# Kernel optimization log

Hardware: AMD Instinct MI355X
Metric: run time of the kernel (lower is better)

The kernel has to match this reference:

```python
import jax, jax.numpy as jnp
import numpy as np

D_MODEL = 1024
D_INNER = 2048      # expand * d_model
D_STATE = 64
HEADDIM = 128
NHEADS = 16         # d_inner // headdim
D_CONV = 4
CHUNK = 256
D_IN_PROJ = 2 * D_INNER + 2 * D_STATE + NHEADS   # 4240 (ngroups=1)
CONV_DIM = D_INNER + 2 * D_STATE                 # 2176
EPS = 1e-5


def setup_inputs() -> dict:
    key = jax.random.key(0)
    ks = jax.random.split(key, 8)
    B, L = 2, 4096
    u = jax.random.normal(ks[0], (B, L, D_MODEL), jnp.float32)
    in_proj_w = jax.random.normal(ks[1], (D_IN_PROJ, D_MODEL), jnp.float32) / np.sqrt(D_MODEL)
    conv_w = jax.random.uniform(ks[2], (CONV_DIM, D_CONV), jnp.float32, -0.5, 0.5)
    conv_b = jnp.zeros((CONV_DIM,), jnp.float32)
    # dt_bias init exactly as in the module: inv-softplus of dt ~ logU(1e-3, 1e-1)
    dt0 = jnp.exp(jax.random.uniform(ks[3], (NHEADS,), jnp.float32) * (np.log(0.1) - np.log(0.001)) + np.log(0.001))
    dt_bias = dt0 + jnp.log(-jnp.expm1(-dt0))
    A_log = jnp.log(jax.random.uniform(ks[4], (NHEADS,), jnp.float32, 1.0, 16.0))
    Dp = jnp.ones((NHEADS,), jnp.float32)
    norm_w = jnp.ones((D_INNER,), jnp.float32)
    out_proj_w = jax.random.normal(ks[5], (D_MODEL, D_INNER), jnp.float32) / np.sqrt(D_INNER)
    return dict(u=u, in_proj_w=in_proj_w, conv_w=conv_w, conv_b=conv_b, dt_bias=dt_bias,
                A_log=A_log, Dp=Dp, norm_w=norm_w, out_proj_w=out_proj_w)


def _ssd(x, dt, A, Bm, Cm, Dp):
    # Chunked selective state-space scan (mamba_chunk_scan_combined semantics).
    # x: [b,l,h,p], dt: [b,l,h] (already softplus'd), A: [h] (negative), Bm/Cm: [b,l,n]
    b, l, h, p = x.shape
    n = Bm.shape[-1]
    nc = l // CHUNK
    xc = x.reshape(b, nc, CHUNK, h, p)
    dtc = dt.reshape(b, nc, CHUNK, h)
    Bc = Bm.reshape(b, nc, CHUNK, n)
    Cc = Cm.reshape(b, nc, CHUNK, n)
    a = dtc * A                       # [b,c,q,h], a <= 0
    acum = jnp.cumsum(a, axis=2)      # within-chunk cumulative log-decay
    # ---- intra-chunk (causal, attention-like) ----
    scores = jnp.einsum('bcqn,bckn->bcqk', Cc, Bc)
    diff = acum[:, :, :, None, :] - acum[:, :, None, :, :]        # [b,c,q,k,h]
    mask = jnp.tril(jnp.ones((CHUNK, CHUNK), bool))[None, None, :, :, None]
    decay = jnp.exp(jnp.where(mask, diff, -jnp.inf))
    M = scores[..., None] * decay * dtc[:, :, None, :, :]         # [b,c,q,k,h]
    y_diag = jnp.einsum('bcqkh,bckhp->bcqhp', M, xc)
    # ---- per-chunk end states ----
    decay_states = jnp.exp(acum[:, :, -1:, :] - acum)             # [b,c,q,h]
    states = jnp.einsum('bcqh,bcqn,bcqhp->bchpn', dtc * decay_states, Bc, xc)
    # ---- inter-chunk recurrence (scan over nc chunks) ----
    chunk_decay = jnp.exp(acum[:, :, -1, :])                      # [b,c,h]
    def step(s, inp):
        st, cd = inp
        return cd[:, :, None, None] * s + st, s                   # emit state BEFORE this chunk
    init = jnp.zeros((b, h, p, n), x.dtype)
    _, prev = jax.lax.scan(step, init, (states.transpose(1, 0, 2, 3, 4), chunk_decay.transpose(1, 0, 2)))
    prev = prev.transpose(1, 0, 2, 3, 4)                          # [b,c,h,p,n]
    y_off = jnp.einsum('bcqn,bchpn,bcqh->bcqhp', Cc, prev, jnp.exp(acum))
    y = y_diag + y_off + xc * Dp[None, None, None, :, None]
    return y.reshape(b, l, h, p)


def _forward(u, in_proj_w, conv_w, conv_b, dt_bias, A_log, Dp, norm_w, out_proj_w):
    b, l, _ = u.shape
    zxbct = jnp.einsum('bld,ed->ble', u, in_proj_w)
    z = zxbct[..., :D_INNER]
    xBC = zxbct[..., D_INNER:D_INNER + CONV_DIM]
    dt = zxbct[..., D_INNER + CONV_DIM:]
    dt = jax.nn.softplus(dt + dt_bias)                            # [b,l,h]
    # causal depthwise conv1d (padding d_conv-1, truncated to seq_len) + SiLU
    xp = jnp.pad(xBC, ((0, 0), (D_CONV - 1, 0), (0, 0)))
    conv_out = conv_b
    for w in range(D_CONV):
        conv_out = conv_out + xp[:, w:w + l, :] * conv_w[:, w]
    xBC = jax.nn.silu(conv_out)
    x = xBC[..., :D_INNER]
    Bm = xBC[..., D_INNER:D_INNER + D_STATE]
    Cm = xBC[..., D_INNER + D_STATE:]
    A = -jnp.exp(A_log)
    y = _ssd(x.reshape(b, l, NHEADS, HEADDIM), dt, A, Bm, Cm, Dp)
    y = y.reshape(b, l, D_INNER)
    # RMSNormGated (norm_before_gate=False): gate first, then RMSNorm
    y = y * jax.nn.silu(z)
    y = y * jax.lax.rsqrt(jnp.mean(y * y, axis=-1, keepdims=True) + EPS) * norm_w
    return jnp.einsum('ble,de->bld', y, out_proj_w)


def reference(u, in_proj_w, conv_w, conv_b, dt_bias, A_log, Dp, norm_w, out_proj_w):
    return _forward(u, in_proj_w, conv_w, conv_b, dt_bias, A_log, Dp, norm_w, out_proj_w)
```

## Files before the change

### kernel.cpp

```cpp
#include <hip/hip_runtime.h>
#include <hip/hip_bf16.h>
#include <cstdint>
#include <cstddef>

#define D_MODEL   1024
#define D_INNER   2048
#define D_STATE   64
#define HEADDIM   128
#define NHEADS    16
#define D_CONV    4
#define CHUNK     256
#define D_IN_PROJ 4240
#define ZPAD      4352
#define CONV_DIM  2176
#define NB        2
#define LEN       4096
#define NC        16
#define MROWS     (NB*LEN)

typedef __hip_bfloat16 bf16;
typedef __bf16 bf16x8 __attribute__((ext_vector_type(8)));
typedef float  f32x4  __attribute__((ext_vector_type(4)));
typedef unsigned short us4 __attribute__((ext_vector_type(4)));

__device__ __forceinline__ float fsilu(float x){ return x / (1.f + __expf(-x)); }
__device__ __forceinline__ float toF(float x){ return x; }
__device__ __forceinline__ float toF(bf16 x){ return __bfloat162float(x); }

__device__ __forceinline__ unsigned short f2bs(float v){
  return __bfloat16_as_ushort(__float2bfloat16(v));
}
__device__ __forceinline__ void store4(bf16* p, f32x4 v){
  us4 o; o[0]=f2bs(v[0]); o[1]=f2bs(v[1]); o[2]=f2bs(v[2]); o[3]=f2bs(v[3]);
  *(us4*)p = o;
}
__device__ __forceinline__ void store4(float* p, f32x4 v){
  *(f32x4*)p = v;
}

__device__ __forceinline__ void gload_lds16(const void* g, void* l){
  __builtin_amdgcn_global_load_lds(
     (const __attribute__((address_space(1))) unsigned int*)(uintptr_t)g,
     (__attribute__((address_space(3))) unsigned int*)(uintptr_t)l, 16, 0, 0);
}

template<typename TC>
__global__ __launch_bounds__(256) void k_gemm_db(
    const bf16* __restrict__ A, int lda,
    const bf16* __restrict__ B, int ldb,
    TC* __restrict__ C, int ldc, int K)
{
  __shared__ __align__(16) __bf16 As[2][128*64];
  __shared__ __align__(16) __bf16 Bs[2][128*64];
  const int tid  = threadIdx.x;
  const int w    = tid >> 6, l = tid & 63;
  const int quad = l >> 4, lq = l & 15;
  const int wm   = (w & 1)*64, wn = (w >> 1)*64;
  const int m0 = blockIdx.x*128, n0 = blockIdx.y*128;

  const int rs = w*8 + (l >> 3);
  const int cs = ((l & 7) ^ (l >> 3)) * 8;
  const bf16* Ag = A + (size_t)(m0 + rs)*lda + cs;
  const bf16* Bg = B + (size_t)(n0 + rs)*ldb + cs;

  auto stage = [&](int t, int buf){
    const int k0 = t*64;
    #pragma unroll
    for (int j=0;j<4;j++){
      gload_lds16(Ag + (size_t)j*32*lda + k0, (char*)&As[buf][0] + (j*32 + w*8)*128);
      gload_lds16(Bg + (size_t)j*32*ldb + k0, (char*)&Bs[buf][0] + (j*32 + w*8)*128);
    }
  };

  f32x4 acc[4][4] = {};

  stage(0, 0);
  const int NT = K >> 6;
  for (int t = 0; t < NT; ++t){
    const int cur = t & 1;
    if (t+1 < NT){
      stage(t+1, cur^1);
      asm volatile("s_waitcnt vmcnt(8)" ::: "memory");
    } else {
      asm volatile("s_waitcnt vmcnt(0)" ::: "memory");
    }
    asm volatile("s_barrier" ::: "memory");

    const char* Ab = (const char*)&As[cur][0];
    const char* Bb = (const char*)&Bs[cur][0];
    #pragma unroll
    for (int s=0;s<2;s++){
      const int slot = ((s*4 + quad) ^ (lq & 7)) << 4;
      bf16x8 af[4], bfr[4];
      #pragma unroll
      for (int tm=0;tm<4;tm++)
        af[tm]  = *(const bf16x8*)(Ab + (wm + lq + tm*16)*128 + slot);
      #pragma unroll
      for (int tn=0;tn<4;tn++)
        bfr[tn] = *(const bf16x8*)(Bb + (wn + lq + tn*16)*128 + slot);
      #pragma unroll
      for (int tm=0;tm<4;tm++)
        #pragma unroll
        for (int tn=0;tn<4;tn++)
          acc[tm][tn] = __builtin_amdgcn_mfma_f32_16x16x32_bf16(bfr[tn], af[tm], acc[tm][tn], 0,0,0);
    }
    asm volatile("s_barrier" ::: "memory");
  }

  #pragma unroll
  for (int tm = 0; tm < 4; tm++){
    int r = m0 + wm + tm*16 + lq;
    #pragma unroll
    for (int tn = 0; tn < 4; tn++){
      int cb = n0 + wn + tn*16 + quad*4;
      store4(&C[(size_t)r*ldc + cb], acc[tm][tn]);
    }
  }
}

#define NU4  (MROWS*D_MODEL/4)
#define NW14 (ZPAD*D_MODEL/4)
#define NW24 (D_MODEL*D_INNER/4)
__global__ __launch_bounds__(256) void k_convert(
    const float* __restrict__ u, const float* __restrict__ Win,
    const float* __restrict__ Wout, const float* __restrict__ norm_w,
    bf16* __restrict__ ub, bf16* __restrict__ Wb_in, bf16* __restrict__ Wb_out){
  int i4 = blockIdx.x*256 + threadIdx.x;
  if (i4 < NU4){
    float4 v = ((const float4*)u)[i4];
    us4 o = {f2bs(v.x), f2bs(v.y), f2bs(v.z), f2bs(v.w)};
    ((us4*)ub)[i4] = o;
  } else if (i4 < NU4 + NW14){
    int j = i4 - NU4;
    int r = j >> 8;
    float4 v = make_float4(0.f,0.f,0.f,0.f);
    if (r < D_IN_PROJ) v = ((const float4*)Win)[j];
    us4 o = {f2bs(v.x), f2bs(v.y), f2bs(v.z), f2bs(v.w)};
    ((us4*)Wb_in)[j] = o;
  } else {
    int j = i4 - NU4 - NW14;
    float4 v = ((const float4*)Wout)[j];
    float4 nw = ((const float4*)norm_w)[j & 511];
    us4 o = {f2bs(v.x*nw.x), f2bs(v.y*nw.y), f2bs(v.z*nw.z), f2bs(v.w*nw.w)};
    ((us4*)Wb_out)[j] = o;
  }
}

__global__ __launch_bounds__(256) void k_dt(
    const bf16* __restrict__ zxbct, const float* __restrict__ dt_bias,
    const float* __restrict__ A_log, float* __restrict__ dt_t,
    float* __restrict__ acum_t, float* __restrict__ cd_t){
  int bid = blockIdx.x;
  int h = bid & 15, c = (bid>>4)&15, b = bid>>8;
  int q = threadIdx.x;
  size_t m = (size_t)(b*NC + c)*CHUNK + q;
  float x = toF(zxbct[m*ZPAD + (D_INNER + CONV_DIM) + h]) + dt_bias[h];
  float dtv = (x > 20.f) ? x : log1pf(__expf(x));
  float Ah = -__expf(A_log[h]);
  float a = dtv * Ah;
  __shared__ float sb[CHUNK];
  sb[q] = a;
  __syncthreads();
  #pragma unroll
  for (int off=1; off<CHUNK; off<<=1){
    float t = (q >= off) ? sb[q-off] : 0.f;
    __syncthreads();
    sb[q] += t;
    __syncthreads();
  }
  float ac = sb[q];
  size_t o = ((size_t)(b*NHEADS+h))*LEN + c*CHUNK + q;
  dt_t[o]   = dtv;
  acum_t[o] = ac;
  if (q == CHUNK-1) cd_t[(b*NHEADS+h)*NC + c] = __expf(ac);
}

__global__ __launch_bounds__(256) void k_conv(
    const bf16* __restrict__ zxbct, const float* __restrict__ conv_w,
    const float* __restrict__ conv_b, bf16* __restrict__ xbc){
  __shared__ __align__(16) __bf16 xs[67*64];
  __shared__ __align__(16) float  ws[64*4];
  __shared__ float bs[64];
  const int tid = threadIdx.x;
  const int cq = tid & 7;
  const int tm = tid >> 3;
  const int c0 = blockIdx.x*64;
  const int m0 = blockIdx.y*64;
  {
    int g = m0 - 3 + tm; if (g < 0) g = 0;
    *(bf16x8*)&xs[tm*64 + cq*8] =
        *(const bf16x8*)(zxbct + (size_t)g*ZPAD + D_INNER + c0 + cq*8);
    int g2 = m0 - 3 + tm + 32;
    *(bf16x8*)&xs[(tm+32)*64 + cq*8] =
        *(const bf16x8*)(zxbct + (size_t)g2*ZPAD + D_INNER + c0 + cq*8);
    if (tid < 24){
      int r3 = 64 + (tid >> 3);
      int g3 = m0 - 3 + r3;
      *(bf16x8*)&xs[r3*64 + cq*8] =
          *(const bf16x8*)(zxbct + (size_t)g3*ZPAD + D_INNER + c0 + cq*8);
    }
  }
  if (tid < 64)      *(float4*)&ws[tid*4] = *(const float4*)(conv_w + (size_t)(c0+tid)*4);
  else if (tid < 128) bs[tid-64] = conv_b[c0 + tid - 64];
  __syncthreads();

  #pragma unroll
  for (int rr=0; rr<2; rr++){
    const int r = tm + rr*32;
    const int m = m0 + r;
    const int l = m & (LEN-1);
    float acc[8];
    #pragma unroll
    for (int j=0;j<8;j++) acc[j] = bs[cq*8+j];
    #pragma unroll
    for (int w=0; w<D_CONV; w++){
      if (l - (D_CONV-1) + w >= 0){
        bf16x8 v = *(const bf16x8*)&xs[(r+w)*64 + cq*8];
        #pragma unroll
        for (int j=0;j<8;j++) acc[j] += (float)v[j] * ws[(cq*8+j)*4 + w];
      }
    }
    bf16x8 o;
    #pragma unroll
    for (int j=0;j<8;j++) o[j] = (__bf16)fsilu(acc[j]);
    *(bf16x8*)(xbc + (size_t)m*CONV_DIM + c0 + cq*8) = o;
  }
}

__global__ __launch_bounds__(256,2) void k_states(
    const bf16* __restrict__ xbc, const float* __restrict__ acum_t,
    const float* __restrict__ dt_t, float* __restrict__ states)
{
  const int bid = blockIdx.x;
  const int h = bid & 15, c = (bid>>4)&15, b = bid>>8;
  const int z = b*NC + c;
  const int tid = threadIdx.x;
  const int w = tid >> 6, l = tid & 63;
  const int quad = l >> 4, lq = l & 15;

  __shared__ __align__(16) __bf16 xsT[2][128*72];
  __shared__ __align__(16) __bf16 bts[2][64*72];

  const float* acum = acum_t + ((size_t)(b*NHEADS+h))*LEN + c*CHUNK;
  const float* dtc  = dt_t   + ((size_t)(b*NHEADS+h))*LEN + c*CHUNK;
  const float alast = acum[CHUNK-1];
  const bf16* xrow = xbc + (size_t)z*CHUNK*CONV_DIM + h*HEADDIM;
  const bf16* Brow = xbc + (size_t)z*CHUNK*CONV_DIM + D_INNER;

  f32x4 Sst[2][4] = {};

  auto stage = [&](int t, int buf){
    const int k0 = t*64;
    const bf16* xr = xrow + (size_t)(k0+l)*CONV_DIM;
    #pragma unroll
    for (int pass=0; pass<4; pass++){
      int pb = w*8 + pass*32;
      bf16x8 v = *(const bf16x8*)(xr + pb);
      #pragma unroll
      for (int j=0;j<8;j++) xsT[buf][(pb+j)*72 + l] = v[j];
    }
    float wl = dtc[k0+l] * __expf(alast - acum[k0+l]);
    const bf16* br = Brow + (size_t)(k0+l)*CONV_DIM;
    #pragma unroll
    for (int pass=0; pass<2; pass++){
      int nb = w*8 + pass*32;
      bf16x8 v = *(const bf16x8*)(br + nb);
      #pragma unroll
      for (int j=0;j<8;j++) bts[buf][(nb+j)*72 + l] = (__bf16)((float)v[j] * wl);
    }
  };

  stage(0, 0);
  for (int t = 0; t < 4; t++){
    const int buf = t & 1;
    __syncthreads();
    if (t < 3) stage(t+1, buf^1);
    #pragma unroll
    for (int s=0;s<2;s++){
      bf16x8 a2[2];
      #pragma unroll
      for (int mi=0;mi<2;mi++)
        a2[mi] = *(const bf16x8*)&xsT[buf][(w*32 + mi*16 + lq)*72 + s*32 + quad*8];
      #pragma unroll
      for (int ni=0;ni<4;ni++){
        bf16x8 bb = *(const bf16x8*)&bts[buf][(ni*16+lq)*72 + s*32 + quad*8];
        #pragma unroll
        for (int mi=0;mi<2;mi++)
          Sst[mi][ni] = __builtin_amdgcn_mfma_f32_16x16x32_bf16(bb, a2[mi], Sst[mi][ni], 0,0,0);
      }
    }
  }

  float* so = states + (size_t)bid*HEADDIM*D_STATE;
  #pragma unroll
  for (int mi=0;mi<2;mi++){
    int pp = w*32 + mi*16 + lq;
    #pragma unroll
    for (int ni=0;ni<4;ni++)
      store4(&so[pp*D_STATE + ni*16 + quad*4], Sst[mi][ni]);
  }
}

__global__ __launch_bounds__(256) void k_scan(
    const float* __restrict__ states, const float* __restrict__ cd_t,
    bf16* __restrict__ prevb){
  int b = blockIdx.x >> 4, h = blockIdx.x & 15;
  int pt = blockIdx.y;
  int tid = threadIdx.x;
  float carry[4] = {0.f,0.f,0.f,0.f};
  for (int c=0;c<NC;c++){
    size_t base = ((size_t)(b*256 + c*16 + h))*HEADDIM*D_STATE + (size_t)pt*1024;
    float cd = cd_t[(b*NHEADS+h)*NC + c];
    #pragma unroll
    for (int i=0;i<4;i++){
      size_t idx = base + (size_t)i*256 + tid;
      prevb[idx] = __float2bfloat16(carry[i]);
      carry[i] = carry[i]*cd + states[idx];
    }
  }
}

__global__ __launch_bounds__(256,2) void k_fused(
    const bf16* __restrict__ xbc, const float* __restrict__ acum_t,
    const float* __restrict__ dt_t, const float* __restrict__ Dp,
    const bf16* __restrict__ prevb, bf16* __restrict__ y)
{
  const int bid = blockIdx.x;
  const int h = bid & 15, c = (bid>>4)&15, b = bid>>8;
  const int z = b*NC + c;
  const int tid = threadIdx.x;
  const int w = tid >> 6, l = tid & 63;
  const int quad = l >> 4, lq = l & 15;

  __shared__ __align__(16) __bf16 xsT[2][128*72];
  __shared__ __align__(16) __bf16 Ms[4][32*40];
  __shared__ float acs[CHUNK], dts[CHUNK];

  const float* acum = acum_t + ((size_t)(b*NHEADS+h))*LEN + c*CHUNK;
  const float* dtc  = dt_t   + ((size_t)(b*NHEADS+h))*LEN + c*CHUNK;
  acs[tid] = acum[tid];
  dts[tid] = dtc[tid];

  const bf16* xrow = xbc + (size_t)z*CHUNK*CONV_DIM + h*HEADDIM;
  const bf16* Brow = xbc + (size_t)z*CHUNK*CONV_DIM + D_INNER;
  const bf16* Crow = xbc + (size_t)z*CHUNK*CONV_DIM + D_INNER + D_STATE;
  const bf16* pv   = prevb + (size_t)bid*HEADDIM*D_STATE;
  const float Dph = Dp[h];
  const int j0 = w, j1 = 7 - w;

  f32x4 Yacc[2][2][8] = {};

  auto stage = [&](int t, int buf){
    const bf16* xr = xrow + (size_t)(t*64+l)*CONV_DIM;
    #pragma unroll
    for (int pass=0; pass<4; pass++){
      int pb = w*8 + pass*32;
      bf16x8 v = *(const bf16x8*)(xr + pb);
      #pragma unroll
      for (int j=0;j<8;j++) xsT[buf][(pb+j)*72 + l] = v[j];
    }
  };

  stage(0, 0);
  __syncthreads();

  #pragma unroll
  for (int s=0;s<2;s++){
    bf16x8 bp[8];
    #pragma unroll
    for (int pn=0;pn<8;pn++)
      bp[pn] = *(const bf16x8*)(pv + (pn*16+lq)*D_STATE + s*32 + quad*8);
    #pragma unroll
    for (int half=0; half<2; half++){
      const int j = half ? j1 : j0;
      #pragma unroll
      for (int qm=0;qm<2;qm++){
        int row = j*32 + qm*16 + lq;
        float e = __expf(acs[row]);
        bf16x8 a = *(const bf16x8*)(Crow + (size_t)row*CONV_DIM + s*32 + quad*8);
        bf16x8 ae;
        #pragma unroll
        for (int jj=0;jj<8;jj++) ae[jj] = (__bf16)((float)a[jj] * e);
        #pragma unroll
        for (int pn=0;pn<8;pn++)
          Yacc[half][qm][pn] = __builtin_amdgcn_mfma_f32_16x16x32_bf16(bp[pn], ae, Yacc[half][qm][pn], 0,0,0);
      }
    }
  }

  for (int t = 0; t < 4; t++){
    const int buf = t & 1;
    if (t > 0) __syncthreads();
    if (t < 3) stage(t+1, buf^1);

    #pragma unroll
    for (int half=0; half<2; half++){
      const int j = half ? j1 : j0;
      if (2*t > j) continue;
      const int qbase = j*32;
      bf16x8 cf[2][2];
      #pragma unroll
      for (int s=0;s<2;s++)
        #pragma unroll
        for (int qm=0;qm<2;qm++)
          cf[s][qm] = *(const bf16x8*)(Crow + (size_t)(qbase+qm*16+lq)*CONV_DIM + s*32 + quad*8);
      #pragma unroll
      for (int kk=0; kk<2; kk++){
        const int kh = 2*t + kk;
        if (kh > j) continue;
        const int kb32  = kk*32;
        const int kbase = kh*32;
        f32x4 Sacc[2][2] = {};
        #pragma unroll
        for (int s=0;s<2;s++){
          bf16x8 bfk[2];
          #pragma unroll
          for (int kn=0;kn<2;kn++)
            bfk[kn] = *(const bf16x8*)(Brow + (size_t)(kbase+kn*16+lq)*CONV_DIM + s*32 + quad*8);
          #pragma unroll
          for (int kn=0;kn<2;kn++)
            #pragma unroll
            for (int qm=0;qm<2;qm++)
              Sacc[kn][qm] = __builtin_amdgcn_mfma_f32_16x16x32_bf16(bfk[kn], cf[s][qm], Sacc[kn][qm], 0,0,0);
        }
        #pragma unroll
        for (int qm=0;qm<2;qm++){
          int ql = qbase + qm*16 + lq;
          float aq = acs[ql];
          #pragma unroll
          for (int kn=0;kn<2;kn++){
            us4 o;
            #pragma unroll
            for (int i=0;i<4;i++){
              int kl = kbase + kn*16 + quad*4 + i;
              float v = Sacc[kn][qm][i] * __expf(aq - acs[kl]) * dts[kl];
              v = (kl < ql) ? v : ((kl == ql) ? v + Dph : 0.f);
              o[i] = f2bs(v);
            }
            *(us4*)&Ms[w][(qm*16+lq)*40 + kn*16 + quad*4] = o;
          }
        }
        asm volatile("s_waitcnt lgkmcnt(0)" ::: "memory");
        #pragma unroll
        for (int qm=0;qm<2;qm++){
          bf16x8 am = *(const bf16x8*)&Ms[w][(qm*16+lq)*40 + quad*8];
          #pragma unroll
          for (int pn=0;pn<8;pn++){
            bf16x8 bp = *(const bf16x8*)&xsT[buf][(pn*16+lq)*72 + kb32 + quad*8];
            Yacc[half][qm][pn] = __builtin_amdgcn_mfma_f32_16x16x32_bf16(bp, am, Yacc[half][qm][pn], 0,0,0);
          }
        }
      }
    }
  }

  bf16* yrow = y + (size_t)z*CHUNK*D_INNER + h*HEADDIM;
  #pragma unroll
  for (int half=0; half<2; half++){
    const int j = half ? j1 : j0;
    #pragma unroll
    for (int qm=0;qm<2;qm++){
      int q = j*32 + qm*16 + lq;
      #pragma unroll
      for (int pn=0;pn<8;pn++)
        store4(&yrow[(size_t)q*D_INNER + pn*16 + quad*4], Yacc[half][qm][pn]);
    }
  }
}

__global__ __launch_bounds__(256) void k_gatenorm(
    const bf16* __restrict__ zxbct, bf16* __restrict__ y){
  int m = blockIdx.x;
  int e0 = threadIdx.x*8;
  bf16x8 zv = *(const bf16x8*)(zxbct + (size_t)m*ZPAD + e0);
  bf16x8 yv = *(const bf16x8*)(y + (size_t)m*D_INNER + e0);
  float v[8]; float ss = 0.f;
  #pragma unroll
  for (int j=0;j<8;j++){
    float val = (float)yv[j] * fsilu((float)zv[j]);
    v[j] = val; ss += val*val;
  }
  #pragma unroll
  for (int off=32; off>0; off>>=1) ss += __shfl_down(ss, off, 64);
  __shared__ float red[4];
  if ((threadIdx.x & 63) == 0) red[threadIdx.x >> 6] = ss;
  __syncthreads();
  float tot = red[0]+red[1]+red[2]+red[3];
  float r = rsqrtf(tot * (1.f/D_INNER) + 1e-5f);
  bf16x8 o;
  #pragma unroll
  for (int j=0;j<8;j++) o[j] = (__bf16)(v[j] * r);
  *(bf16x8*)(y + (size_t)m*D_INNER + e0) = o;
}

extern "C" void kernel_launch(void* const* d_in, const int* in_sizes, int n_in,
                              void* d_out, int out_size, void* d_ws, size_t ws_size,
                              hipStream_t stream) {
  const float* u         = (const float*)d_in[0];
  const float* in_proj_w = (const float*)d_in[1];
  const float* conv_w    = (const float*)d_in[2];
  const float* conv_b    = (const float*)d_in[3];
  const float* dt_bias   = (const float*)d_in[4];
  const float* A_log     = (const float*)d_in[5];
  const float* Dp        = (const float*)d_in[6];
  const float* norm_w    = (const float*)d_in[7];
  const float* out_proj_w= (const float*)d_in[8];
  float* out = (float*)d_out;

  char* p = (char*)d_ws;
  auto alloc = [&](size_t bytes){ char* r = p; p += (bytes + 255) & ~size_t(255); return r; };
  bf16*  zxbct = (bf16*) alloc((size_t)MROWS*ZPAD*2);
  bf16*  xbc   = (bf16*) alloc((size_t)MROWS*CONV_DIM*2);
  bf16*  y     = (bf16*) alloc((size_t)MROWS*D_INNER*2);
  bf16*  ub    = (bf16*) alloc((size_t)MROWS*D_MODEL*2);
  bf16*  Wb_in = (bf16*) alloc((size_t)ZPAD*D_MODEL*2);
  bf16*  Wb_out= (bf16*) alloc((size_t)D_MODEL*D_INNER*2);
  float* dt_t  = (float*)alloc((size_t)NB*NHEADS*LEN*4);
  float* acum_t= (float*)alloc((size_t)NB*NHEADS*LEN*4);
  float* cd_t  = (float*)alloc((size_t)NB*NHEADS*NC*4);
  float* states= (float*)ub;
  bf16*  prevb = (bf16*)Wb_in;

  dim3 blk(256);
  k_convert<<<dim3((NU4+NW14+NW24)/256), blk, 0, stream>>>(
      u, in_proj_w, out_proj_w, norm_w, ub, Wb_in, Wb_out);

  k_gemm_db<bf16><<<dim3(64, 34), blk, 0, stream>>>(
      ub, D_MODEL, Wb_in, D_MODEL, zxbct, ZPAD, D_MODEL);

  k_dt    <<<dim3(NB*NC*NHEADS), blk, 0, stream>>>(zxbct, dt_bias, A_log, dt_t, acum_t, cd_t);
  k_conv  <<<dim3(CONV_DIM/64, MROWS/64), blk, 0, stream>>>(zxbct, conv_w, conv_b, xbc);
  k_states<<<dim3(NB*NC*NHEADS), blk, 0, stream>>>(xbc, acum_t, dt_t, states);
  k_scan  <<<dim3(NB*NHEADS, 8), blk, 0, stream>>>(states, cd_t, prevb);
  k_fused <<<dim3(NB*NC*NHEADS), blk, 0, stream>>>(xbc, acum_t, dt_t, Dp, prevb, y);
  k_gatenorm<<<dim3(MROWS), blk, 0, stream>>>(zxbct, y);

  k_gemm_db<float><<<dim3(64, 8), blk, 0, stream>>>(
      y, D_INNER, Wb_out, D_INNER, out, D_MODEL, D_INNER);
}
```

Before: 344.4 us.

## Run GEMM tiles with eight waves per block and hoist C fragments in fused SSD kernel

Both GEMMs now run with 512 threads per block instead of 256. Each wave computes a 64x32 sub-tile instead of 64x64, and the LDS staging is reindexed so each thread issues four 16-byte global-to-LDS loads per K step. The goal is more waves for latency hiding and fewer accumulator registers per wave. Separately, the fused SSD kernel loads its C-matrix fragments once into registers and reuses them across the state pass and every intra-chunk step, instead of reloading them from global memory each time. This costs more resident registers in that kernel.

```diff
diff --git a/kernel.cpp b/kernel.cpp
--- a/kernel.cpp
+++ b/kernel.cpp
@@ -45,7 +45,7 @@
 }
 
 template<typename TC>
-__global__ __launch_bounds__(256) void k_gemm_db(
+__global__ __launch_bounds__(512) void k_gemm_8w(
     const bf16* __restrict__ A, int lda,
     const bf16* __restrict__ B, int ldb,
     TC* __restrict__ C, int ldc, int K)
@@ -55,24 +55,27 @@
   const int tid  = threadIdx.x;
   const int w    = tid >> 6, l = tid & 63;
   const int quad = l >> 4, lq = l & 15;
-  const int wm   = (w & 1)*64, wn = (w >> 1)*64;
+  const int wm   = (w & 1)*64;
+  const int wn   = (w >> 1)*32;
   const int m0 = blockIdx.x*128, n0 = blockIdx.y*128;
 
-  const int rs = w*8 + (l >> 3);
-  const int cs = ((l & 7) ^ (l >> 3)) * 8;
-  const bf16* Ag = A + (size_t)(m0 + rs)*lda + cs;
-  const bf16* Bg = B + (size_t)(n0 + rs)*ldb + cs;
+  const int sr = tid >> 3;
+  const int sc = ((tid & 7) ^ (sr & 7)) * 8;
+  const bf16* Ag = A + (size_t)(m0 + sr)*lda + sc;
+  const bf16* Bg = B + (size_t)(n0 + sr)*ldb + sc;
+  const int sdo = w*1024;
 
   auto stage = [&](int t, int buf){
     const int k0 = t*64;
-    #pragma unroll
-    for (int j=0;j<4;j++){
-      gload_lds16(Ag + (size_t)j*32*lda + k0, (char*)&As[buf][0] + (j*32 + w*8)*128);
-      gload_lds16(Bg + (size_t)j*32*ldb + k0, (char*)&Bs[buf][0] + (j*32 + w*8)*128);
-    }
+    char* ab = (char*)&As[buf][0] + sdo;
+    char* bb = (char*)&Bs[buf][0] + sdo;
+    gload_lds16(Ag + k0,                  ab);
+    gload_lds16(Ag + (size_t)64*lda + k0, ab + 8192);
+    gload_lds16(Bg + k0,                  bb);
+    gload_lds16(Bg + (size_t)64*ldb + k0, bb + 8192);
   };
 
-  f32x4 acc[4][4] = {};
+  f32x4 acc[4][2] = {};
 
   stage(0, 0);
   const int NT = K >> 6;
@@ -80,7 +83,7 @@
     const int cur = t & 1;
     if (t+1 < NT){
       stage(t+1, cur^1);
-      asm volatile("s_waitcnt vmcnt(8)" ::: "memory");
+      asm volatile("s_waitcnt vmcnt(4)" ::: "memory");
     } else {
       asm volatile("s_waitcnt vmcnt(0)" ::: "memory");
     }
@@ -90,18 +93,18 @@
     const char* Bb = (const char*)&Bs[cur][0];
     #pragma unroll
     for (int s=0;s<2;s++){
-      const int slot = ((s*4 + quad) ^ (lq & 7)) << 4;
-      bf16x8 af[4], bfr[4];
+      const int slot = (((s*4 + quad) ^ (lq & 7)) << 4);
+      bf16x8 af[4], bfr[2];
       #pragma unroll
       for (int tm=0;tm<4;tm++)
-        af[tm]  = *(const bf16x8*)(Ab + (wm + lq + tm*16)*128 + slot);
-      #pragma unroll
-      for (int tn=0;tn<4;tn++)
-        bfr[tn] = *(const bf16x8*)(Bb + (wn + lq + tn*16)*128 + slot);
+        af[tm]  = *(const bf16x8*)(Ab + (wm + tm*16 + lq)*128 + slot);
+      #pragma unroll
+      for (int tn=0;tn<2;tn++)
+        bfr[tn] = *(const bf16x8*)(Bb + (wn + tn*16 + lq)*128 + slot);
       #pragma unroll
       for (int tm=0;tm<4;tm++)
         #pragma unroll
-        for (int tn=0;tn<4;tn++)
+        for (int tn=0;tn<2;tn++)
           acc[tm][tn] = __builtin_amdgcn_mfma_f32_16x16x32_bf16(bfr[tn], af[tm], acc[tm][tn], 0,0,0);
     }
     asm volatile("s_barrier" ::: "memory");
@@ -111,7 +114,7 @@
   for (int tm = 0; tm < 4; tm++){
     int r = m0 + wm + tm*16 + lq;
     #pragma unroll
-    for (int tn = 0; tn < 4; tn++){
+    for (int tn = 0; tn < 2; tn++){
       int cb = n0 + wn + tn*16 + quad*4;
       store4(&C[(size_t)r*ldc + cb], acc[tm][tn]);
     }
@@ -362,6 +365,18 @@
   };
 
   stage(0, 0);
+
+  bf16x8 cfh[2][2][2];
+  #pragma unroll
+  for (int half=0; half<2; half++){
+    const int j = half ? j1 : j0;
+    #pragma unroll
+    for (int s=0;s<2;s++)
+      #pragma unroll
+      for (int qm=0;qm<2;qm++)
+        cfh[half][s][qm] = *(const bf16x8*)(Crow + (size_t)(j*32+qm*16+lq)*CONV_DIM + s*32 + quad*8);
+  }
+
   __syncthreads();
 
   #pragma unroll
@@ -377,7 +392,7 @@
       for (int qm=0;qm<2;qm++){
         int row = j*32 + qm*16 + lq;
         float e = __expf(acs[row]);
-        bf16x8 a = *(const bf16x8*)(Crow + (size_t)row*CONV_DIM + s*32 + quad*8);
+        bf16x8 a = cfh[half][s][qm];
         bf16x8 ae;
         #pragma unroll
         for (int jj=0;jj<8;jj++) ae[jj] = (__bf16)((float)a[jj] * e);
@@ -398,12 +413,6 @@
       const int j = half ? j1 : j0;
       if (2*t > j) continue;
       const int qbase = j*32;
-      bf16x8 cf[2][2];
-      #pragma unroll
-      for (int s=0;s<2;s++)
-        #pragma unroll
-        for (int qm=0;qm<2;qm++)
-          cf[s][qm] = *(const bf16x8*)(Crow + (size_t)(qbase+qm*16+lq)*CONV_DIM + s*32 + quad*8);
       #pragma unroll
       for (int kk=0; kk<2; kk++){
         const int kh = 2*t + kk;
@@ -421,7 +430,7 @@
           for (int kn=0;kn<2;kn++)
             #pragma unroll
             for (int qm=0;qm<2;qm++)
-              Sacc[kn][qm] = __builtin_amdgcn_mfma_f32_16x16x32_bf16(bfk[kn], cf[s][qm], Sacc[kn][qm], 0,0,0);
+              Sacc[kn][qm] = __builtin_amdgcn_mfma_f32_16x16x32_bf16(bfk[kn], cfh[half][s][qm], Sacc[kn][qm], 0,0,0);
         }
         #pragma unroll
         for (int qm=0;qm<2;qm++){
@@ -525,7 +534,7 @@
   k_convert<<<dim3((NU4+NW14+NW24)/256), blk, 0, stream>>>(
       u, in_proj_w, out_proj_w, norm_w, ub, Wb_in, Wb_out);
 
-  k_gemm_db<bf16><<<dim3(64, 34), blk, 0, stream>>>(
+  k_gemm_8w<bf16><<<dim3(64, 34), dim3(512), 0, stream>>>(
       ub, D_MODEL, Wb_in, D_MODEL, zxbct, ZPAD, D_MODEL);
 
   k_dt    <<<dim3(NB*NC*NHEADS), blk, 0, stream>>>(zxbct, dt_bias, A_log, dt_t, acum_t, cd_t);
@@ -535,6 +544,6 @@
   k_fused <<<dim3(NB*NC*NHEADS), blk, 0, stream>>>(xbc, acum_t, dt_t, Dp, prevb, y);
   k_gatenorm<<<dim3(MROWS), blk, 0, stream>>>(zxbct, y);
 
-  k_gemm_db<float><<<dim3(64, 8), blk, 0, stream>>>(
+  k_gemm_8w<float><<<dim3(64, 8), dim3(512), 0, stream>>>(
       y, D_INNER, Wb_out, D_INNER, out, D_MODEL, D_INNER);
 }
```

New measurement: 346.2 us. About the same (+0.5%).
